# Optimization experiments

Measured on AMD Instinct MI355X. Metric: run time of the kernel, lower is better.

## Reference

```python
import jax, jax.numpy as jnp
import numpy as np

N = 100000      # nodes
E = 3200000     # directed edges
G = 1024        # graphs in batch


def setup_inputs() -> dict:
    key = jax.random.key(0)
    ks = jax.random.split(key, 12)
    x = jax.random.normal(ks[0], (N, 4), dtype=jnp.float32)
    edge_index = jax.random.randint(ks[1], (2, E), 0, N, dtype=jnp.int64)
    batch = jnp.sort(jax.random.randint(ks[2], (N,), 0, G, dtype=jnp.int64))
    s = 0.1
    return {
        'x': x, 'edge_index': edge_index, 'batch': batch,
        'W_emb': jax.random.normal(ks[3], (4, 1), jnp.float32) * s,
        'b_emb': jax.random.normal(ks[4], (4,), jnp.float32) * s,
        'W1': jax.random.normal(ks[5], (16, 7), jnp.float32) * s,
        'b1': jax.random.normal(ks[6], (16,), jnp.float32) * s,
        'W2': jax.random.normal(ks[7], (8, 16), jnp.float32) * s,
        'b2': jax.random.normal(ks[8], (8,), jnp.float32) * s,
        'W3': jax.random.normal(ks[9], (1, 8), jnp.float32) * s,
        'b3': jax.random.normal(ks[10], (1,), jnp.float32) * s,
    }


def _gcn_norm(edge_index, n):
    # add self-loops (PyG GCNConv default)
    loops = jnp.arange(n, dtype=edge_index.dtype)
    row = jnp.concatenate([edge_index[0], loops])  # source
    col = jnp.concatenate([edge_index[1], loops])  # target
    deg = jax.ops.segment_sum(jnp.ones_like(col, dtype=jnp.float32), col, num_segments=n)
    dinv = jnp.where(deg > 0, deg ** -0.5, 0.0)
    norm = dinv[row] * dinv[col]
    return row, col, norm


def _gcn_conv(h, W, b, row, col, norm, n):
    h = h @ W.T                                   # [n, out]
    msg = h[row] * norm[:, None]                  # gather + scale
    out = jax.ops.segment_sum(msg, col, num_segments=n)
    return out + b


def reference(x, edge_index, batch, W_emb, b_emb, W1, b1, W2, b2, W3, b3):
    row, col, norm = _gcn_norm(edge_index, N)
    atoms_vector = x[:, :1]
    atoms_xyz = x[:, 1:]
    one_hot_emb = atoms_vector @ W_emb.T + b_emb          # [N, 4]
    h = jnp.concatenate([one_hot_emb, atoms_xyz], axis=1) # [N, 7]
    h = jnp.tanh(_gcn_conv(h, W1, b1, row, col, norm, N)) # [N, 16]
    # dropout is identity in eval mode
    h = jnp.tanh(_gcn_conv(h, W2, b2, row, col, norm, N)) # [N, 8]
    # scatter-mean readout over graphs
    sums = jax.ops.segment_sum(h, batch, num_segments=G)
    cnts = jax.ops.segment_sum(jnp.ones((h.shape[0],), h.dtype), batch, num_segments=G)
    pooled = sums / jnp.maximum(cnts, 1.0)[:, None]       # [G, 8]
    return pooled @ W3.T + b3                             # [G, 1]
```

## Files before the change

### kernel.cpp

```cpp
#include <hip/hip_runtime.h>
#include <hip/hip_fp16.h>


constexpr int BLK  = 256;
constexpr int NPB  = 256;
constexpr int NBMX = 512;
constexpr int CAPB = 9216;
constexpr int CAPS = 5120;
constexpr int EPT  = CAPS / BLK;
constexpr int SBLK = 512;
constexpr int MAXIT = CAPB / SBLK;

__global__ void k_place(const int4* __restrict__ row4, const int4* __restrict__ col4,
                        int* __restrict__ bucketCnt, unsigned int* __restrict__ data,
                        int E, int NB) {
    __shared__ unsigned int stage[CAPS];
    __shared__ int pos[NBMX], sstart[NBMX], lbase[NBMX];
    __shared__ int wsum[4];
    int t = threadIdx.x;
    int lane = t & 63, w = t >> 6;
    int begin = blockIdx.x * CAPS;
    int end = min(E, begin + CAPS);
    int csize = end - begin;
    int q0 = begin >> 2, q1 = end >> 2;
    for (int i = t; i < NBMX; i += BLK) pos[i] = 0;
    __syncthreads();
    unsigned int ent[EPT];
    int meta[EPT];
#pragma unroll
    for (int it = 0; it < EPT / 4; it++) {
        int i = q0 + t + it * BLK;
        bool ok = i < q1;
        int4 c = ok ? col4[i] : make_int4(0, 0, 0, 0);
        int4 r = ok ? row4[i] : make_int4(0, 0, 0, 0);
#pragma unroll
        for (int k = 0; k < 4; k++) {
            int cc = ((const int*)&c)[k];
            int rr = ((const int*)&r)[k];
            int b = cc >> 8;
            int o = ok ? atomicAdd(&pos[b], 1) : 0;
            ent[it * 4 + k] = ((unsigned int)(cc & 255) << 17) | (unsigned int)rr;
            meta[it * 4 + k] = ok ? ((b << 13) | o) : -1;
        }
    }
    __syncthreads();
    int b0 = 2 * t, b1 = 2 * t + 1;
    int h0 = pos[b0], h1 = pos[b1];
    int tsum = h0 + h1;
    int sc = tsum;
#pragma unroll
    for (int off = 1; off < 64; off <<= 1) {
        int o = __shfl_up(sc, off, 64);
        if (lane >= off) sc += o;
    }
    if (lane == 63) wsum[w] = sc;
    __syncthreads();
    int pre = 0;
#pragma unroll
    for (int i = 0; i < 4; i++) if (i < w) pre += wsum[i];
    int excl = sc + pre - tsum;
    sstart[b0] = excl;
    sstart[b1] = excl + h0;
    lbase[b0] = h0 ? atomicAdd(&bucketCnt[b0], h0) : 0;
    lbase[b1] = h1 ? atomicAdd(&bucketCnt[b1], h1) : 0;
    __syncthreads();
#pragma unroll
    for (int k = 0; k < EPT; k++) {
        int m = meta[k];
        if (m >= 0) stage[sstart[m >> 13] + (m & 0x1FFF)] = ent[k];
    }
    __syncthreads();
    for (int k = t; k < csize; k += BLK) {
        int lo = 0, hi = NB - 1;
        while (lo < hi) { int m = (lo + hi + 1) >> 1; if (sstart[m] <= k) lo = m; else hi = m - 1; }
        data[(unsigned int)lo * CAPB + (unsigned int)(lbase[lo] + (k - sstart[lo]))] = stage[k];
    }
}

__global__ void k_sort_node1(unsigned int* __restrict__ data,
                             const int* __restrict__ bucketCnt,
                             const float4* __restrict__ x,
                             const float* __restrict__ Wemb, const float* __restrict__ bemb,
                             const float* __restrict__ W1,
                             int* __restrict__ rs, int* __restrict__ re,
                             float* __restrict__ dinv, uint4* __restrict__ u1q, int n) {
    __shared__ int pos[NPB], startl[NPB];
    __shared__ int wsum[4];
    int b = blockIdx.x;
    int t = threadIdx.x;
    int base = b * CAPB;
    int cnt = min(bucketCnt[b], CAPB);
    if (t < NPB) pos[t] = 0;
    __syncthreads();
    unsigned int ent[MAXIT];
    int off[MAXIT];
#pragma unroll
    for (int it = 0; it < MAXIT; it++) {
        int i = t + it * SBLK;
        if (i < cnt) {
            unsigned int p = data[base + i];
            int dloc = (int)(p >> 17);
            int o = atomicAdd(&pos[dloc], 1);
            ent[it] = p & 0x1FFFF;
            off[it] = (dloc << 14) | o;
        } else off[it] = -1;
    }
    __syncthreads();
    int node = b * NPB + t;
    float d = 0.0f;
    int v = 0;
    if (t < NPB) {
        int lane = t & 63, w = t >> 6;
        v = pos[t];
        int sc = v;
#pragma unroll
        for (int o = 1; o < 64; o <<= 1) {
            int s = __shfl_up(sc, o, 64);
            if (lane >= o) sc += s;
        }
        if (lane == 63) wsum[w] = sc;
        __syncthreads();
        int pre = 0;
#pragma unroll
        for (int i = 0; i < 4; i++) if (i < w) pre += wsum[i];
        int excl = sc + pre - v;
        startl[t] = excl;
        if (node < n) {
            rs[node] = base + excl;
            re[node] = base + excl + v;
            d = rsqrtf((float)v + 1.0f);
            dinv[node] = d;
        }
    } else {
        __syncthreads();
    }
    __syncthreads();
#pragma unroll
    for (int it = 0; it < MAXIT; it++) {
        int m = off[it];
        if (m >= 0) data[base + startl[m >> 14] + (m & 0x3FFF)] = ent[it];
    }
    if (t < NPB && node < n) {
        float4 xi = x[node];
        float h0[7];
#pragma unroll
        for (int j = 0; j < 4; j++) h0[j] = xi.x * Wemb[j] + bemb[j];
        h0[4] = xi.y; h0[5] = xi.z; h0[6] = xi.w;
        float s[16];
#pragma unroll
        for (int f = 0; f < 16; f++) {
            float tt = 0.0f;
#pragma unroll
            for (int j = 0; j < 7; j++) tt += h0[j] * W1[f * 7 + j];
            s[f] = tt * d;
        }
        union { __half2 h2[8]; uint4 u4[2]; } pk;
#pragma unroll
        for (int q = 0; q < 8; q++) pk.h2[q] = __floats2half2_rn(s[2*q], s[2*q+1]);
        u1q[node * 2]     = pk.u4[0];
        u1q[node * 2 + 1] = pk.u4[1];
    }
}

__global__ void k_agg1(const unsigned int* __restrict__ sorted,
                       const int* __restrict__ rs, const int* __restrict__ re,
                       const __half2* __restrict__ u1h2, const float* __restrict__ dinv,
                       const float* __restrict__ b1, const float* __restrict__ W2,
                       __half* __restrict__ u2h, int n) {
    __shared__ float hbuf[32][17];
    int nl = threadIdx.x >> 3;
    int f = threadIdx.x & 7;
    int node = blockIdx.x * 32 + nl;
    if (node < n) {
        int s = rs[node], e = re[node];
        float2 acc = make_float2(0.0f, 0.0f);
        int j = s;
        for (; j + 4 <= e; j += 4) {
            int r0 = sorted[j], r1 = sorted[j+1], r2 = sorted[j+2], r3 = sorted[j+3];
            float2 a0 = __half22float2(u1h2[r0 * 8 + f]);
            float2 a1 = __half22float2(u1h2[r1 * 8 + f]);
            float2 a2 = __half22float2(u1h2[r2 * 8 + f]);
            float2 a3 = __half22float2(u1h2[r3 * 8 + f]);
            acc.x += (a0.x + a1.x) + (a2.x + a3.x);
            acc.y += (a0.y + a1.y) + (a2.y + a3.y);
        }
        for (; j < e; j++) {
            float2 a = __half22float2(u1h2[sorted[j] * 8 + f]);
            acc.x += a.x; acc.y += a.y;
        }
        float2 self = __half22float2(u1h2[node * 8 + f]);
        float d = dinv[node];
        hbuf[nl][2*f]   = tanhf(d * (acc.x + self.x) + b1[2*f]);
        hbuf[nl][2*f+1] = tanhf(d * (acc.y + self.y) + b1[2*f+1]);
    }
    __syncthreads();
    int nl2 = threadIdx.x >> 3;
    int g = threadIdx.x & 7;
    int node2 = blockIdx.x * 32 + nl2;
    if (node2 < n) {
        float t = 0.0f;
#pragma unroll
        for (int j = 0; j < 16; j++) t += hbuf[nl2][j] * W2[g * 16 + j];
        u2h[node2 * 8 + g] = __float2half(t * dinv[node2]);
    }
}

__global__ void k_agg2(const unsigned int* __restrict__ sorted,
                       const int* __restrict__ rs, const int* __restrict__ re,
                       const __half2* __restrict__ u2h2, const float* __restrict__ dinv,
                       const float* __restrict__ b2, __half2* __restrict__ h2h2, int n) {
    int node = blockIdx.x * 64 + (threadIdx.x >> 2);
    int f = threadIdx.x & 3;
    if (node >= n) return;
    int s = rs[node], e = re[node];
    float2 acc = make_float2(0.0f, 0.0f);
    int j = s;
    for (; j + 4 <= e; j += 4) {
        int r0 = sorted[j], r1 = sorted[j+1], r2 = sorted[j+2], r3 = sorted[j+3];
        float2 a0 = __half22float2(u2h2[r0 * 4 + f]);
        float2 a1 = __half22float2(u2h2[r1 * 4 + f]);
        float2 a2 = __half22float2(u2h2[r2 * 4 + f]);
        float2 a3 = __half22float2(u2h2[r3 * 4 + f]);
        acc.x += (a0.x + a1.x) + (a2.x + a3.x);
        acc.y += (a0.y + a1.y) + (a2.y + a3.y);
    }
    for (; j < e; j++) {
        float2 a = __half22float2(u2h2[sorted[j] * 4 + f]);
        acc.x += a.x; acc.y += a.y;
    }
    float2 self = __half22float2(u2h2[node * 4 + f]);
    float d = dinv[node];
    h2h2[node * 4 + f] = __floats2half2_rn(tanhf(d * (acc.x + self.x) + b2[2*f]),
                                           tanhf(d * (acc.y + self.y) + b2[2*f+1]));
}

__global__ void k_pool_out(const uint4* __restrict__ h2q, const int* __restrict__ batch,
                           const float* __restrict__ W3, const float* __restrict__ b3,
                           float* __restrict__ out, int n) {
    int g = blockIdx.x;
    int lane = threadIdx.x;
    int lo = 0, hi = n;
    while (lo < hi) { int m = (lo + hi) >> 1; if (batch[m] < g) lo = m + 1; else hi = m; }
    int start = lo;
    hi = n;
    while (lo < hi) { int m = (lo + hi) >> 1; if (batch[m] < g + 1) lo = m + 1; else hi = m; }
    int end = lo;

    float s[8];
#pragma unroll
    for (int f = 0; f < 8; f++) s[f] = 0.0f;
    for (int i = start + lane; i < end; i += 64) {
        uint4 q = h2q[i];
        const __half2* ph = (const __half2*)&q;
#pragma unroll
        for (int p = 0; p < 4; p++) {
            float2 a = __half22float2(ph[p]);
            s[2*p]   += a.x;
            s[2*p+1] += a.y;
        }
    }
#pragma unroll
    for (int off = 32; off >= 1; off >>= 1) {
#pragma unroll
        for (int f = 0; f < 8; f++) s[f] += __shfl_down(s[f], off, 64);
    }
    if (lane == 0) {
        float c = fmaxf((float)(end - start), 1.0f);
        float t = 0.0f;
#pragma unroll
        for (int f = 0; f < 8; f++) t += (s[f] / c) * W3[f];
        out[g] = t + b3[0];
    }
}

extern "C" void kernel_launch(void* const* d_in, const int* in_sizes, int n_in,
                              void* d_out, int out_size, void* d_ws, size_t ws_size,
                              hipStream_t stream) {
    const float* x    = (const float*)d_in[0];
    const int*   ei   = (const int*)d_in[1];
    const int*   batch= (const int*)d_in[2];
    const float* Wemb = (const float*)d_in[3];
    const float* bemb = (const float*)d_in[4];
    const float* W1   = (const float*)d_in[5];
    const float* b1   = (const float*)d_in[6];
    const float* W2   = (const float*)d_in[7];
    const float* b2   = (const float*)d_in[8];
    const float* W3   = (const float*)d_in[9];
    const float* b3   = (const float*)d_in[10];
    float* out = (float*)d_out;

    const int n = in_sizes[2];
    const int E = in_sizes[1] / 2;
    const int G = out_size;
    const int* row = ei;
    const int* col = ei + E;
    const int NB = (n + NPB - 1) / NPB;

    float* ws    = (float*)d_ws;
    float* dinv  = ws;
    uint4* u1q   = (uint4*)(ws + n);
    __half* u2h  = (__half*)(ws + 9 * n);
    __half* h2h  = (__half*)(ws + 13 * n);
    int* rs      = (int*)(ws + 17 * n);
    int* re      = rs + n;
    int* bucketCnt = re + n;
    unsigned int* data = (unsigned int*)(bucketCnt + NBMX);

    int gridP = (E + CAPS - 1) / CAPS;

    hipMemsetAsync(bucketCnt, 0, NBMX * sizeof(int), stream);
    k_place<<<gridP, BLK, 0, stream>>>((const int4*)row, (const int4*)col,
                                       bucketCnt, data, E, NB);
    k_sort_node1<<<NB, SBLK, 0, stream>>>(data, bucketCnt, (const float4*)x,
                                          Wemb, bemb, W1, rs, re, dinv, u1q, n);
    k_agg1<<<(n + 31) / 32, BLK, 0, stream>>>(data, rs, re, (const __half2*)u1q,
                                              dinv, b1, W2, u2h, n);
    k_agg2<<<(n + 63) / 64, BLK, 0, stream>>>(data, rs, re, (const __half2*)u2h,
                                              dinv, b2, (__half2*)h2h, n);
    k_pool_out<<<G, 64, 0, stream>>>((const uint4*)h2h, batch, W3, b3, out, n);
}
```

Before: 219.0 us.

## Widen per-thread gathers in aggregation kernels and enlarge placement blocks

The aggregation kernels now gather each neighbour's features as one wide vector per thread instead of splitting features across 8 or 4 lanes. In agg1 two threads cover a node with 16-byte loads, and in agg2 one thread covers a node with a single 16-byte load. This cuts the number of index loads and memory transactions per edge, at the cost of more per-thread serial work and more load imbalance between threads within a wavefront. The placement kernel moves to 512 threads with one bucket per thread and a larger chunk per block, which simplifies the scan and reduces the block count.

```diff
diff --git a/kernel.cpp b/kernel.cpp
--- a/kernel.cpp
+++ b/kernel.cpp
@@ -6,8 +6,9 @@
 constexpr int NPB  = 256;
 constexpr int NBMX = 512;
 constexpr int CAPB = 9216;
-constexpr int CAPS = 5120;
-constexpr int EPT  = CAPS / BLK;
+constexpr int PBLK = 512;
+constexpr int CAPS = 6144;
+constexpr int EPT  = 12;
 constexpr int SBLK = 512;
 constexpr int MAXIT = CAPB / SBLK;
 
@@ -16,20 +17,20 @@
                         int E, int NB) {
     __shared__ unsigned int stage[CAPS];
     __shared__ int pos[NBMX], sstart[NBMX], lbase[NBMX];
-    __shared__ int wsum[4];
+    __shared__ int wsum[8];
     int t = threadIdx.x;
     int lane = t & 63, w = t >> 6;
     int begin = blockIdx.x * CAPS;
     int end = min(E, begin + CAPS);
     int csize = end - begin;
     int q0 = begin >> 2, q1 = end >> 2;
-    for (int i = t; i < NBMX; i += BLK) pos[i] = 0;
+    if (t < NBMX) pos[t] = 0;
     __syncthreads();
     unsigned int ent[EPT];
     int meta[EPT];
 #pragma unroll
     for (int it = 0; it < EPT / 4; it++) {
-        int i = q0 + t + it * BLK;
+        int i = q0 + t + it * PBLK;
         bool ok = i < q1;
         int4 c = ok ? col4[i] : make_int4(0, 0, 0, 0);
         int4 r = ok ? row4[i] : make_int4(0, 0, 0, 0);
@@ -44,10 +45,8 @@
         }
     }
     __syncthreads();
-    int b0 = 2 * t, b1 = 2 * t + 1;
-    int h0 = pos[b0], h1 = pos[b1];
-    int tsum = h0 + h1;
-    int sc = tsum;
+    int v = pos[t];
+    int sc = v;
 #pragma unroll
     for (int off = 1; off < 64; off <<= 1) {
         int o = __shfl_up(sc, off, 64);
@@ -57,12 +56,10 @@
     __syncthreads();
     int pre = 0;
 #pragma unroll
-    for (int i = 0; i < 4; i++) if (i < w) pre += wsum[i];
-    int excl = sc + pre - tsum;
-    sstart[b0] = excl;
-    sstart[b1] = excl + h0;
-    lbase[b0] = h0 ? atomicAdd(&bucketCnt[b0], h0) : 0;
-    lbase[b1] = h1 ? atomicAdd(&bucketCnt[b1], h1) : 0;
+    for (int i = 0; i < 8; i++) if (i < w) pre += wsum[i];
+    int excl = sc + pre - v;
+    sstart[t] = excl;
+    lbase[t] = v ? atomicAdd(&bucketCnt[t], v) : 0;
     __syncthreads();
 #pragma unroll
     for (int k = 0; k < EPT; k++) {
@@ -70,7 +67,7 @@
         if (m >= 0) stage[sstart[m >> 13] + (m & 0x1FFF)] = ent[k];
     }
     __syncthreads();
-    for (int k = t; k < csize; k += BLK) {
+    for (int k = t; k < csize; k += PBLK) {
         int lo = 0, hi = NB - 1;
         while (lo < hi) { int m = (lo + hi + 1) >> 1; if (sstart[m] <= k) lo = m; else hi = m - 1; }
         data[(unsigned int)lo * CAPB + (unsigned int)(lbase[lo] + (k - sstart[lo]))] = stage[k];
@@ -108,10 +105,9 @@
     __syncthreads();
     int node = b * NPB + t;
     float d = 0.0f;
-    int v = 0;
     if (t < NPB) {
         int lane = t & 63, w = t >> 6;
-        v = pos[t];
+        int v = pos[t];
         int sc = v;
 #pragma unroll
         for (int o = 1; o < 64; o <<= 1) {
@@ -164,74 +160,122 @@
 
 __global__ void k_agg1(const unsigned int* __restrict__ sorted,
                        const int* __restrict__ rs, const int* __restrict__ re,
-                       const __half2* __restrict__ u1h2, const float* __restrict__ dinv,
+                       const uint4* __restrict__ u1q, const float* __restrict__ dinv,
                        const float* __restrict__ b1, const float* __restrict__ W2,
-                       __half* __restrict__ u2h, int n) {
-    __shared__ float hbuf[32][17];
-    int nl = threadIdx.x >> 3;
-    int f = threadIdx.x & 7;
-    int node = blockIdx.x * 32 + nl;
+                       uint2* __restrict__ u2h, int n) {
+    __shared__ float hbuf[128][17];
+    int t = threadIdx.x;
+    int nl = t >> 1;
+    int j = t & 1;
+    int node = blockIdx.x * 128 + nl;
     if (node < n) {
         int s = rs[node], e = re[node];
-        float2 acc = make_float2(0.0f, 0.0f);
-        int j = s;
-        for (; j + 4 <= e; j += 4) {
-            int r0 = sorted[j], r1 = sorted[j+1], r2 = sorted[j+2], r3 = sorted[j+3];
-            float2 a0 = __half22float2(u1h2[r0 * 8 + f]);
-            float2 a1 = __half22float2(u1h2[r1 * 8 + f]);
-            float2 a2 = __half22float2(u1h2[r2 * 8 + f]);
-            float2 a3 = __half22float2(u1h2[r3 * 8 + f]);
-            acc.x += (a0.x + a1.x) + (a2.x + a3.x);
-            acc.y += (a0.y + a1.y) + (a2.y + a3.y);
-        }
-        for (; j < e; j++) {
-            float2 a = __half22float2(u1h2[sorted[j] * 8 + f]);
-            acc.x += a.x; acc.y += a.y;
-        }
-        float2 self = __half22float2(u1h2[node * 8 + f]);
+        float acc[8];
+#pragma unroll
+        for (int k = 0; k < 8; k++) acc[k] = 0.0f;
+        int i = s;
+        for (; i + 4 <= e; i += 4) {
+            uint4 q0 = u1q[sorted[i]     * 2 + j];
+            uint4 q1 = u1q[sorted[i + 1] * 2 + j];
+            uint4 q2 = u1q[sorted[i + 2] * 2 + j];
+            uint4 q3 = u1q[sorted[i + 3] * 2 + j];
+            const __half2* p0 = (const __half2*)&q0;
+            const __half2* p1 = (const __half2*)&q1;
+            const __half2* p2 = (const __half2*)&q2;
+            const __half2* p3 = (const __half2*)&q3;
+#pragma unroll
+            for (int k = 0; k < 4; k++) {
+                float2 a0 = __half22float2(p0[k]);
+                float2 a1 = __half22float2(p1[k]);
+                float2 a2 = __half22float2(p2[k]);
+                float2 a3 = __half22float2(p3[k]);
+                acc[2*k]   += (a0.x + a1.x) + (a2.x + a3.x);
+                acc[2*k+1] += (a0.y + a1.y) + (a2.y + a3.y);
+            }
+        }
+        for (; i < e; i++) {
+            uint4 q = u1q[sorted[i] * 2 + j];
+            const __half2* p = (const __half2*)&q;
+#pragma unroll
+            for (int k = 0; k < 4; k++) {
+                float2 a = __half22float2(p[k]);
+                acc[2*k]   += a.x;
+                acc[2*k+1] += a.y;
+            }
+        }
+        uint4 qs = u1q[node * 2 + j];
+        const __half2* ps = (const __half2*)&qs;
         float d = dinv[node];
-        hbuf[nl][2*f]   = tanhf(d * (acc.x + self.x) + b1[2*f]);
-        hbuf[nl][2*f+1] = tanhf(d * (acc.y + self.y) + b1[2*f+1]);
-    }
-    __syncthreads();
-    int nl2 = threadIdx.x >> 3;
-    int g = threadIdx.x & 7;
-    int node2 = blockIdx.x * 32 + nl2;
-    if (node2 < n) {
-        float t = 0.0f;
-#pragma unroll
-        for (int j = 0; j < 16; j++) t += hbuf[nl2][j] * W2[g * 16 + j];
-        u2h[node2 * 8 + g] = __float2half(t * dinv[node2]);
+#pragma unroll
+        for (int k = 0; k < 4; k++) {
+            float2 a = __half22float2(ps[k]);
+            hbuf[nl][j*8 + 2*k]   = tanhf(d * (acc[2*k]   + a.x) + b1[j*8 + 2*k]);
+            hbuf[nl][j*8 + 2*k+1] = tanhf(d * (acc[2*k+1] + a.y) + b1[j*8 + 2*k+1]);
+        }
+    }
+    __syncthreads();
+    if (node < n) {
+        float d = dinv[node];
+        float r[4];
+#pragma unroll
+        for (int gg = 0; gg < 4; gg++) {
+            float tt = 0.0f;
+#pragma unroll
+            for (int k = 0; k < 16; k++) tt += hbuf[nl][k] * W2[(j*4 + gg) * 16 + k];
+            r[gg] = tt * d;
+        }
+        union { __half2 h2[2]; uint2 u2; } pk;
+        pk.h2[0] = __floats2half2_rn(r[0], r[1]);
+        pk.h2[1] = __floats2half2_rn(r[2], r[3]);
+        u2h[node * 2 + j] = pk.u2;
     }
 }
 
 __global__ void k_agg2(const unsigned int* __restrict__ sorted,
                        const int* __restrict__ rs, const int* __restrict__ re,
-                       const __half2* __restrict__ u2h2, const float* __restrict__ dinv,
-                       const float* __restrict__ b2, __half2* __restrict__ h2h2, int n) {
-    int node = blockIdx.x * 64 + (threadIdx.x >> 2);
-    int f = threadIdx.x & 3;
+                       const uint4* __restrict__ u2q, const float* __restrict__ dinv,
+                       const float* __restrict__ b2, uint4* __restrict__ h2q, int n) {
+    int node = blockIdx.x * BLK + threadIdx.x;
     if (node >= n) return;
     int s = rs[node], e = re[node];
-    float2 acc = make_float2(0.0f, 0.0f);
-    int j = s;
-    for (; j + 4 <= e; j += 4) {
-        int r0 = sorted[j], r1 = sorted[j+1], r2 = sorted[j+2], r3 = sorted[j+3];
-        float2 a0 = __half22float2(u2h2[r0 * 4 + f]);
-        float2 a1 = __half22float2(u2h2[r1 * 4 + f]);
-        float2 a2 = __half22float2(u2h2[r2 * 4 + f]);
-        float2 a3 = __half22float2(u2h2[r3 * 4 + f]);
-        acc.x += (a0.x + a1.x) + (a2.x + a3.x);
-        acc.y += (a0.y + a1.y) + (a2.y + a3.y);
-    }
-    for (; j < e; j++) {
-        float2 a = __half22float2(u2h2[sorted[j] * 4 + f]);
-        acc.x += a.x; acc.y += a.y;
-    }
-    float2 self = __half22float2(u2h2[node * 4 + f]);
+    float acc[8];
+#pragma unroll
+    for (int k = 0; k < 8; k++) acc[k] = 0.0f;
+    int i = s;
+    for (; i + 2 <= e; i += 2) {
+        uint4 q0 = u2q[sorted[i]];
+        uint4 q1 = u2q[sorted[i + 1]];
+        const __half2* p0 = (const __half2*)&q0;
+        const __half2* p1 = (const __half2*)&q1;
+#pragma unroll
+        for (int k = 0; k < 4; k++) {
+            float2 a0 = __half22float2(p0[k]);
+            float2 a1 = __half22float2(p1[k]);
+            acc[2*k]   += a0.x + a1.x;
+            acc[2*k+1] += a0.y + a1.y;
+        }
+    }
+    if (i < e) {
+        uint4 q = u2q[sorted[i]];
+        const __half2* p = (const __half2*)&q;
+#pragma unroll
+        for (int k = 0; k < 4; k++) {
+            float2 a = __half22float2(p[k]);
+            acc[2*k]   += a.x;
+            acc[2*k+1] += a.y;
+        }
+    }
+    uint4 qs = u2q[node];
+    const __half2* ps = (const __half2*)&qs;
     float d = dinv[node];
-    h2h2[node * 4 + f] = __floats2half2_rn(tanhf(d * (acc.x + self.x) + b2[2*f]),
-                                           tanhf(d * (acc.y + self.y) + b2[2*f+1]));
+    union { __half2 h2[4]; uint4 u4; } pk;
+#pragma unroll
+    for (int k = 0; k < 4; k++) {
+        float2 a = __half22float2(ps[k]);
+        pk.h2[k] = __floats2half2_rn(tanhf(d * (acc[2*k]   + a.x) + b2[2*k]),
+                                     tanhf(d * (acc[2*k+1] + a.y) + b2[2*k+1]));
+    }
+    h2q[node] = pk.u4;
 }
 
 __global__ void k_pool_out(const uint4* __restrict__ h2q, const int* __restrict__ batch,
@@ -309,13 +353,13 @@
     int gridP = (E + CAPS - 1) / CAPS;
 
     hipMemsetAsync(bucketCnt, 0, NBMX * sizeof(int), stream);
-    k_place<<<gridP, BLK, 0, stream>>>((const int4*)row, (const int4*)col,
-                                       bucketCnt, data, E, NB);
+    k_place<<<gridP, PBLK, 0, stream>>>((const int4*)row, (const int4*)col,
+                                        bucketCnt, data, E, NB);
     k_sort_node1<<<NB, SBLK, 0, stream>>>(data, bucketCnt, (const float4*)x,
                                           Wemb, bemb, W1, rs, re, dinv, u1q, n);
-    k_agg1<<<(n + 31) / 32, BLK, 0, stream>>>(data, rs, re, (const __half2*)u1q,
-                                              dinv, b1, W2, u2h, n);
-    k_agg2<<<(n + 63) / 64, BLK, 0, stream>>>(data, rs, re, (const __half2*)u2h,
-                                              dinv, b2, (__half2*)h2h, n);
+    k_agg1<<<(n + 127) / 128, BLK, 0, stream>>>(data, rs, re, u1q,
+                                                dinv, b1, W2, (uint2*)u2h, n);
+    k_agg2<<<(n + BLK - 1) / BLK, BLK, 0, stream>>>(data, rs, re, (const uint4*)u2h,
+                                                    dinv, b2, (uint4*)h2h, n);
     k_pool_out<<<G, 64, 0, stream>>>((const uint4*)h2h, batch, W3, b3, out, n);
 }
```

Measured after the change: 209.6 us. 4.3% less time.
